# Kernel tuning notes

Measured on AMD Instinct MI355X. Metric: run time of the kernel, lower is better.

The kernel has to match this reference:

```python
import jax, jax.numpy as jnp
import numpy as np


def setup_inputs() -> dict:
    key = jax.random.key(0)
    k1, k2, k3, k4 = jax.random.split(key, 4)
    T, C, D, DY = 8192, 8192, 64, 32
    z_context = jax.random.normal(k1, (C, D), dtype=jnp.float32)
    y_context = jax.random.normal(k2, (C, DY), dtype=jnp.float32)
    z_target = jax.random.normal(k3, (T, D), dtype=jnp.float32)
    # W ~ Uniform(-0.1, 0.1), matching torch init
    W = jax.random.uniform(k4, (D, D), dtype=jnp.float32, minval=-0.1, maxval=0.1)
    return {"z_context": z_context, "y_context": y_context, "z_target": z_target, "W": W}


def _interp(z_context, y_context, z_target, W):
    # score(t,c) = (z_t - z_c)^T W (z_t - z_c), expanded algebraically to avoid
    # the O(T*C*D) pairwise-difference intermediate:
    #   = z_t W z_t + z_c W z_c - z_t W z_c - z_c W z_t
    zt_W = z_target @ W            # (T, D)
    zc_W = z_context @ W           # (C, D)
    q_tt = jnp.sum(zt_W * z_target, axis=-1)   # (T,)
    q_cc = jnp.sum(zc_W * z_context, axis=-1)   # (C,)
    cross = zt_W @ z_context.T + z_target @ zc_W.T  # (T, C): z_t W z_c + z_c W z_t
    scores = q_tt[:, None] + q_cc[None, :] - cross  # (T, C)
    thetas = jnp.exp(-scores)                        # (T, C)
    # weighted sum of context values, normalized per target
    return (thetas @ y_context) / jnp.sum(thetas, axis=-1, keepdims=True)  # (T, DY)


def reference(z_context, y_context, z_target, W):
    return _interp(z_context, y_context, z_target, W)
```

## Files before the change

### kernel.cpp

```cpp
#include <hip/hip_runtime.h>
#include <hip/hip_bf16.h>


typedef float f32x4 __attribute__((ext_vector_type(4)));
typedef __bf16 bf16x8 __attribute__((ext_vector_type(8)));

#define LOG2E 1.4426950408889634f

static __device__ __forceinline__ unsigned short f2bf(float x) {
  unsigned u = __float_as_uint(x);
  u += 0x7fffu + ((u >> 16) & 1u);
  return (unsigned short)(u >> 16);
}
static __device__ __forceinline__ float bf2f(unsigned short h) {
  return __uint_as_float(((unsigned)h) << 16);
}
static __device__ __forceinline__ bf16x8 ldg8(const unsigned short* p) {
  uint4 u = *reinterpret_cast<const uint4*>(p);
  return __builtin_bit_cast(bf16x8, u);
}
static __device__ __forceinline__ unsigned cvt_pk_bf16(float lo, float hi) {
  unsigned r;
  asm("v_cvt_pk_bf16_f32 %0, %1, %2" : "=v"(r) : "v"(lo), "v"(hi));
  return r;
}
static __device__ __forceinline__ void gl2lds(const unsigned short* g, unsigned short* l) {
  __builtin_amdgcn_global_load_lds(
      (const __attribute__((address_space(1))) unsigned int*)g,
      (__attribute__((address_space(3))) unsigned int*)l, 16, 0, 0);
}

__global__ void msym_kernel(const float* __restrict__ W, float* __restrict__ Msym) {
  int idx = blockIdx.x * 256 + threadIdx.x;
  int k = idx >> 6, d = idx & 63;
  Msym[idx] = LOG2E * (W[k * 64 + d] + W[d * 64 + k]);
}

__global__ void prep_kernel(const float* __restrict__ zc, const float* __restrict__ yc,
                            const float* __restrict__ zt, const float* __restrict__ Msym,
                            unsigned short* __restrict__ Qh, unsigned short* __restrict__ Ql,
                            unsigned short* __restrict__ Kh, unsigned short* __restrict__ Kl,
                            unsigned short* __restrict__ Vt, float* __restrict__ bias)
{
  int b = blockIdx.x, tid = threadIdx.x;
  if (b < 2048) {
    int idx = b * 256 + tid;
    int t = idx >> 6, d = idx & 63;
    const float* z = zt + t * 64;
    float q = 0.f;
    #pragma unroll 8
    for (int k = 0; k < 64; ++k) q = fmaf(z[k], Msym[k * 64 + d], q);
    unsigned short h = f2bf(q);
    Qh[idx] = h;
    Ql[idx] = f2bf(q - bf2f(h));
  } else if (b < 4096) {
    int idx = (b - 2048) * 256 + tid;
    float v = zc[idx];
    unsigned short h = f2bf(v);
    Kh[idx] = h;
    Kl[idx] = f2bf(v - bf2f(h));
  } else if (b < 6144) {
    int c = (b - 4096) * 4 + (tid >> 6), j = tid & 63;
    const float* z = zc + c * 64;
    float cs = 0.f;
    #pragma unroll 8
    for (int i = 0; i < 64; ++i) cs = fmaf(z[i], Msym[i * 64 + j], cs);
    float part = cs * z[j];
    #pragma unroll
    for (int off = 32; off >= 1; off >>= 1) part += __shfl_xor(part, off, 64);
    if (j == 0) bias[c] = -0.5f * part;
  } else {
    __shared__ float vt[256][33];
    int cbase = (b - 6144) * 256;
    #pragma unroll
    for (int k = 0; k < 32; ++k) {
      int e = k * 256 + tid;
      vt[e >> 5][e & 31] = yc[cbase * 32 + e];
    }
    __syncthreads();
    #pragma unroll
    for (int k = 0; k < 32; ++k)
      Vt[k * 8192 + cbase + tid] = f2bf(vt[tid][k]);
  }
}


#define STAGE(C0) { \
  const int C0_ = (C0); \
  _Pragma("unroll") \
  for (int i2 = 0; i2 < 2; ++i2) { \
    int i = wid + i2 * 8;                        \
    int row = i * 8 + (lane >> 3); \
    int lchunk = (lane & 7) ^ (lane >> 3); \
    gl2lds(Kh + (C0_ + row) * 64 + lchunk * 8, &KhL[i * 512]); \
    gl2lds(Kl + (C0_ + row) * 64 + lchunk * 8, &KlL[i * 512]); \
  } \
  { \
    int row = wid * 4 + (lane >> 4);             \
    int lchunk = (lane & 15) ^ (row & 15); \
    gl2lds(Vt + row * 8192 + C0_ + lchunk * 8, &VL[wid * 512]); \
  } }

__global__ __launch_bounds__(512, 2) void attn_kernel(
    const unsigned short* __restrict__ Qh, const unsigned short* __restrict__ Ql,
    const unsigned short* __restrict__ Kh, const unsigned short* __restrict__ Kl,
    const unsigned short* __restrict__ Vt, const float* __restrict__ bias,
    float* __restrict__ outAcc, float* __restrict__ denA)
{
  __shared__ unsigned short KhL[128 * 64];
  __shared__ unsigned short KlL[128 * 64];
  __shared__ unsigned short VL[32 * 128];
  __shared__ __align__(16) uint2 p_lds[8][16][34];

  const int tid = threadIdx.x;
  const int wid = tid >> 6, lane = tid & 63;
  const int lr = lane & 15, g = lane >> 4;
  const int tt = blockIdx.x >> 3, cq = blockIdx.x & 7;
  const int tbase = tt * 128 + wid * 16;
  const int cqbase = cq * 1024;

  bf16x8 qh[2], ql[2];
  #pragma unroll
  for (int f = 0; f < 2; ++f) {
    int off = (tbase + lr) * 64 + f * 32 + 8 * g;
    qh[f] = ldg8(Qh + off);
    ql[f] = ldg8(Ql + off);
  }

  uint4 ones_bits = make_uint4(0x3F803F80u, 0x3F803F80u, 0x3F803F80u, 0x3F803F80u);
  bf16x8 vones = __builtin_bit_cast(bf16x8, ones_bits);

  f32x4 acc[2];
  f32x4 den;
  acc[0] = (f32x4)(0.0f);
  acc[1] = (f32x4)(0.0f);
  den = (f32x4)(0.0f);

  for (int st = 0; st < 8; ++st) {
    STAGE(cqbase + st * 128)
    __syncthreads();

    const int cbias = cqbase + st * 128;

    #pragma unroll
    for (int cb = 0; cb < 8; ++cb) {
      int row = cb * 16 + lr;
      int phys0 = g ^ (row & 7);
      int phys1 = (4 + g) ^ (row & 7);
      int off0 = row * 64 + phys0 * 8;
      int off1 = row * 64 + phys1 * 8;
      bf16x8 kh0 = __builtin_bit_cast(bf16x8, *reinterpret_cast<const uint4*>(&KhL[off0]));
      bf16x8 kl0 = __builtin_bit_cast(bf16x8, *reinterpret_cast<const uint4*>(&KlL[off0]));
      bf16x8 kh1 = __builtin_bit_cast(bf16x8, *reinterpret_cast<const uint4*>(&KhL[off1]));
      bf16x8 kl1 = __builtin_bit_cast(bf16x8, *reinterpret_cast<const uint4*>(&KlL[off1]));
      f32x4 sv = (f32x4)(0.0f);
      sv = __builtin_amdgcn_mfma_f32_16x16x32_bf16(kh0, qh[0], sv, 0, 0, 0);
      sv = __builtin_amdgcn_mfma_f32_16x16x32_bf16(kl0, qh[0], sv, 0, 0, 0);
      sv = __builtin_amdgcn_mfma_f32_16x16x32_bf16(kh0, ql[0], sv, 0, 0, 0);
      sv = __builtin_amdgcn_mfma_f32_16x16x32_bf16(kh1, qh[1], sv, 0, 0, 0);
      sv = __builtin_amdgcn_mfma_f32_16x16x32_bf16(kl1, qh[1], sv, 0, 0, 0);
      sv = __builtin_amdgcn_mfma_f32_16x16x32_bf16(kh1, ql[1], sv, 0, 0, 0);
      f32x4 bv = *reinterpret_cast<const f32x4*>(bias + cbias + cb * 16 + 4 * g);
      float p0 = __builtin_amdgcn_exp2f(sv[0] + bv[0]);
      float p1 = __builtin_amdgcn_exp2f(sv[1] + bv[1]);
      float p2 = __builtin_amdgcn_exp2f(sv[2] + bv[2]);
      float p3 = __builtin_amdgcn_exp2f(sv[3] + bv[3]);
      uint2 w2;
      w2.x = cvt_pk_bf16(p0, p1);
      w2.y = cvt_pk_bf16(p2, p3);
      p_lds[wid][lr][cb * 4 + g] = w2;
    }

    #pragma unroll
    for (int ks = 0; ks < 4; ++ks) {
      uint2 ra = p_lds[wid][lr][ks * 8 + 2 * g];
      uint2 rb = p_lds[wid][lr][ks * 8 + 2 * g + 1];
      bf16x8 pa = __builtin_bit_cast(bf16x8, make_uint4(ra.x, ra.y, rb.x, rb.y));
      #pragma unroll
      for (int dyb = 0; dyb < 2; ++dyb) {
        int row = dyb * 16 + lr;
        int phys = (ks * 4 + g) ^ lr;
        bf16x8 vf = __builtin_bit_cast(bf16x8, *reinterpret_cast<const uint4*>(&VL[row * 128 + phys * 8]));
        acc[dyb] = __builtin_amdgcn_mfma_f32_16x16x32_bf16(pa, vf, acc[dyb], 0, 0, 0);
      }
      den = __builtin_amdgcn_mfma_f32_16x16x32_bf16(pa, vones, den, 0, 0, 0);
    }

    __syncthreads();
  }

  #pragma unroll
  for (int dyb = 0; dyb < 2; ++dyb)
    #pragma unroll
    for (int r = 0; r < 4; ++r)
      atomicAdd(&outAcc[(tbase + 4 * g + r) * 32 + dyb * 16 + lr], acc[dyb][r]);
  if (lr == 0) {
    #pragma unroll
    for (int r = 0; r < 4; ++r)
      atomicAdd(&denA[tbase + 4 * g + r], den[r]);
  }
}

__global__ void divide_kernel(float* __restrict__ out, const float* __restrict__ denA)
{
  int i = blockIdx.x * 256 + threadIdx.x;
  out[i] = out[i] / denA[i >> 5];
}

extern "C" void kernel_launch(void* const* d_in, const int* in_sizes, int n_in,
                              void* d_out, int out_size, void* d_ws, size_t ws_size,
                              hipStream_t stream)
{
  const float* zc = (const float*)d_in[0];
  const float* yc = (const float*)d_in[1];
  const float* zt = (const float*)d_in[2];
  const float* W  = (const float*)d_in[3];

  unsigned short* Qh = (unsigned short*)d_ws;
  unsigned short* Ql = Qh + 8192 * 64;
  unsigned short* Kh = Ql + 8192 * 64;
  unsigned short* Kl = Kh + 8192 * 64;
  unsigned short* Vt = Kl + 8192 * 64;
  float* bias = (float*)(Vt + 32 * 8192);
  float* Msym = bias + 8192;
  float* denA = Msym + 4096;
  float* out  = (float*)d_out;

  hipMemsetAsync(out, 0, 8192 * 32 * sizeof(float), stream);
  hipMemsetAsync(denA, 0, 8192 * sizeof(float), stream);
  msym_kernel<<<16, 256, 0, stream>>>(W, Msym);
  prep_kernel<<<6176, 256, 0, stream>>>(zc, yc, zt, Msym, Qh, Ql, Kh, Kl, Vt, bias);
  attn_kernel<<<512, 512, 0, stream>>>(Qh, Ql, Kh, Kl, Vt, bias, out, denA);
  divide_kernel<<<1024, 256, 0, stream>>>(out, denA);
}
```

Before: 72.56 us.

## Switch attention kernel to 32x32 MFMA tiles with register-shuffled probabilities

```diff
diff --git a/kernel.cpp b/kernel.cpp
--- a/kernel.cpp
+++ b/kernel.cpp
@@ -3,6 +3,7 @@
 
 
 typedef float f32x4 __attribute__((ext_vector_type(4)));
+typedef float f32x16 __attribute__((ext_vector_type(16)));
 typedef __bf16 bf16x8 __attribute__((ext_vector_type(8)));
 
 #define LOG2E 1.4426950408889634f
@@ -101,7 +102,7 @@
     gl2lds(Vt + row * 8192 + C0_ + lchunk * 8, &VL[wid * 512]); \
   } }
 
-__global__ __launch_bounds__(512, 2) void attn_kernel(
+__global__ __launch_bounds__(512, 4) void attn_kernel(
     const unsigned short* __restrict__ Qh, const unsigned short* __restrict__ Ql,
     const unsigned short* __restrict__ Kh, const unsigned short* __restrict__ Kl,
     const unsigned short* __restrict__ Vt, const float* __restrict__ bias,
@@ -110,95 +111,112 @@
   __shared__ unsigned short KhL[128 * 64];
   __shared__ unsigned short KlL[128 * 64];
   __shared__ unsigned short VL[32 * 128];
-  __shared__ __align__(16) uint2 p_lds[8][16][34];
 
   const int tid = threadIdx.x;
   const int wid = tid >> 6, lane = tid & 63;
-  const int lr = lane & 15, g = lane >> 4;
-  const int tt = blockIdx.x >> 3, cq = blockIdx.x & 7;
-  const int tbase = tt * 128 + wid * 16;
-  const int cqbase = cq * 1024;
-
-  bf16x8 qh[2], ql[2];
+  const int lm = lane & 31, h = lane >> 5;
+  const int tt = blockIdx.x >> 4, cq = blockIdx.x & 15;
+  const int tbase = tt * 256 + wid * 32;
+  const int cqbase = cq * 512;
+
+  bf16x8 qh[4], ql[4];
   #pragma unroll
-  for (int f = 0; f < 2; ++f) {
-    int off = (tbase + lr) * 64 + f * 32 + 8 * g;
-    qh[f] = ldg8(Qh + off);
-    ql[f] = ldg8(Ql + off);
-  }
-
-  uint4 ones_bits = make_uint4(0x3F803F80u, 0x3F803F80u, 0x3F803F80u, 0x3F803F80u);
-  bf16x8 vones = __builtin_bit_cast(bf16x8, ones_bits);
-
-  f32x4 acc[2];
-  f32x4 den;
-  acc[0] = (f32x4)(0.0f);
-  acc[1] = (f32x4)(0.0f);
-  den = (f32x4)(0.0f);
-
-  for (int st = 0; st < 8; ++st) {
+  for (int kk = 0; kk < 4; ++kk) {
+    int off = (tbase + lm) * 64 + kk * 16 + 8 * h;
+    qh[kk] = ldg8(Qh + off);
+    ql[kk] = ldg8(Ql + off);
+  }
+
+  f32x16 acc = (f32x16)(0.0f);
+  float den = 0.f;
+
+  for (int st = 0; st < 4; ++st) {
     STAGE(cqbase + st * 128)
     __syncthreads();
 
     const int cbias = cqbase + st * 128;
 
     #pragma unroll
-    for (int cb = 0; cb < 8; ++cb) {
-      int row = cb * 16 + lr;
-      int phys0 = g ^ (row & 7);
-      int phys1 = (4 + g) ^ (row & 7);
-      int off0 = row * 64 + phys0 * 8;
-      int off1 = row * 64 + phys1 * 8;
-      bf16x8 kh0 = __builtin_bit_cast(bf16x8, *reinterpret_cast<const uint4*>(&KhL[off0]));
-      bf16x8 kl0 = __builtin_bit_cast(bf16x8, *reinterpret_cast<const uint4*>(&KlL[off0]));
-      bf16x8 kh1 = __builtin_bit_cast(bf16x8, *reinterpret_cast<const uint4*>(&KhL[off1]));
-      bf16x8 kl1 = __builtin_bit_cast(bf16x8, *reinterpret_cast<const uint4*>(&KlL[off1]));
-      f32x4 sv = (f32x4)(0.0f);
-      sv = __builtin_amdgcn_mfma_f32_16x16x32_bf16(kh0, qh[0], sv, 0, 0, 0);
-      sv = __builtin_amdgcn_mfma_f32_16x16x32_bf16(kl0, qh[0], sv, 0, 0, 0);
-      sv = __builtin_amdgcn_mfma_f32_16x16x32_bf16(kh0, ql[0], sv, 0, 0, 0);
-      sv = __builtin_amdgcn_mfma_f32_16x16x32_bf16(kh1, qh[1], sv, 0, 0, 0);
-      sv = __builtin_amdgcn_mfma_f32_16x16x32_bf16(kl1, qh[1], sv, 0, 0, 0);
-      sv = __builtin_amdgcn_mfma_f32_16x16x32_bf16(kh1, ql[1], sv, 0, 0, 0);
-      f32x4 bv = *reinterpret_cast<const f32x4*>(bias + cbias + cb * 16 + 4 * g);
-      float p0 = __builtin_amdgcn_exp2f(sv[0] + bv[0]);
-      float p1 = __builtin_amdgcn_exp2f(sv[1] + bv[1]);
-      float p2 = __builtin_amdgcn_exp2f(sv[2] + bv[2]);
-      float p3 = __builtin_amdgcn_exp2f(sv[3] + bv[3]);
-      uint2 w2;
-      w2.x = cvt_pk_bf16(p0, p1);
-      w2.y = cvt_pk_bf16(p2, p3);
-      p_lds[wid][lr][cb * 4 + g] = w2;
+    for (int cb = 0; cb < 4; ++cb) {
+      const int crow = cb * 32 + lm;
+
+      f32x16 sv = (f32x16)(0.0f);
+      #pragma unroll
+      for (int kk = 0; kk < 4; ++kk) {
+        int phys = (2 * kk + h) ^ (lm & 7);
+        int offr = crow * 64 + phys * 8;
+        bf16x8 kh = __builtin_bit_cast(bf16x8, *reinterpret_cast<const uint4*>(&KhL[offr]));
+        bf16x8 kl = __builtin_bit_cast(bf16x8, *reinterpret_cast<const uint4*>(&KlL[offr]));
+        sv = __builtin_amdgcn_mfma_f32_32x32x16_bf16(kh, qh[kk], sv, 0, 0, 0);
+        sv = __builtin_amdgcn_mfma_f32_32x32x16_bf16(kl, qh[kk], sv, 0, 0, 0);
+        sv = __builtin_amdgcn_mfma_f32_32x32x16_bf16(kh, ql[kk], sv, 0, 0, 0);
+      }
+
+      uint2 own0, own1, own2, own3;
+      float psum;
+      {
+        f32x4 bv0 = *reinterpret_cast<const f32x4*>(bias + cbias + cb * 32 + 0 * 8 + 4 * h);
+        f32x4 bv1 = *reinterpret_cast<const f32x4*>(bias + cbias + cb * 32 + 1 * 8 + 4 * h);
+        f32x4 bv2 = *reinterpret_cast<const f32x4*>(bias + cbias + cb * 32 + 2 * 8 + 4 * h);
+        f32x4 bv3 = *reinterpret_cast<const f32x4*>(bias + cbias + cb * 32 + 3 * 8 + 4 * h);
+        float p00 = __builtin_amdgcn_exp2f(sv[0]  + bv0[0]);
+        float p01 = __builtin_amdgcn_exp2f(sv[1]  + bv0[1]);
+        float p02 = __builtin_amdgcn_exp2f(sv[2]  + bv0[2]);
+        float p03 = __builtin_amdgcn_exp2f(sv[3]  + bv0[3]);
+        float p10 = __builtin_amdgcn_exp2f(sv[4]  + bv1[0]);
+        float p11 = __builtin_amdgcn_exp2f(sv[5]  + bv1[1]);
+        float p12 = __builtin_amdgcn_exp2f(sv[6]  + bv1[2]);
+        float p13 = __builtin_amdgcn_exp2f(sv[7]  + bv1[3]);
+        float p20 = __builtin_amdgcn_exp2f(sv[8]  + bv2[0]);
+        float p21 = __builtin_amdgcn_exp2f(sv[9]  + bv2[1]);
+        float p22 = __builtin_amdgcn_exp2f(sv[10] + bv2[2]);
+        float p23 = __builtin_amdgcn_exp2f(sv[11] + bv2[3]);
+        float p30 = __builtin_amdgcn_exp2f(sv[12] + bv3[0]);
+        float p31 = __builtin_amdgcn_exp2f(sv[13] + bv3[1]);
+        float p32 = __builtin_amdgcn_exp2f(sv[14] + bv3[2]);
+        float p33 = __builtin_amdgcn_exp2f(sv[15] + bv3[3]);
+        psum = ((p00 + p01) + (p02 + p03)) + ((p10 + p11) + (p12 + p13))
+             + ((p20 + p21) + (p22 + p23)) + ((p30 + p31) + (p32 + p33));
+        own0.x = cvt_pk_bf16(p00, p01); own0.y = cvt_pk_bf16(p02, p03);
+        own1.x = cvt_pk_bf16(p10, p11); own1.y = cvt_pk_bf16(p12, p13);
+        own2.x = cvt_pk_bf16(p20, p21); own2.y = cvt_pk_bf16(p22, p23);
+        own3.x = cvt_pk_bf16(p30, p31); own3.y = cvt_pk_bf16(p32, p33);
+      }
+      den += psum;
+
+      unsigned s1x = h ? own0.x : own1.x, s1y = h ? own0.y : own1.y;
+      unsigned s2x = h ? own2.x : own3.x, s2y = h ? own2.y : own3.y;
+      unsigned r1x = __shfl_xor((int)s1x, 32, 64);
+      unsigned r1y = __shfl_xor((int)s1y, 32, 64);
+      unsigned r2x = __shfl_xor((int)s2x, 32, 64);
+      unsigned r2y = __shfl_xor((int)s2y, 32, 64);
+      uint4 f0 = h ? make_uint4(r1x, r1y, own1.x, own1.y)
+                   : make_uint4(own0.x, own0.y, r1x, r1y);
+      uint4 f1 = h ? make_uint4(r2x, r2y, own3.x, own3.y)
+                   : make_uint4(own2.x, own2.y, r2x, r2y);
+
+      {
+        int physv0 = (cb * 4 + 0 * 2 + h) ^ (lm & 15);
+        bf16x8 vf0 = __builtin_bit_cast(bf16x8, *reinterpret_cast<const uint4*>(&VL[lm * 128 + physv0 * 8]));
+        bf16x8 pa0 = __builtin_bit_cast(bf16x8, f0);
+        acc = __builtin_amdgcn_mfma_f32_32x32x16_bf16(pa0, vf0, acc, 0, 0, 0);
+        int physv1 = (cb * 4 + 1 * 2 + h) ^ (lm & 15);
+        bf16x8 vf1 = __builtin_bit_cast(bf16x8, *reinterpret_cast<const uint4*>(&VL[lm * 128 + physv1 * 8]));
+        bf16x8 pa1 = __builtin_bit_cast(bf16x8, f1);
+        acc = __builtin_amdgcn_mfma_f32_32x32x16_bf16(pa1, vf1, acc, 0, 0, 0);
+      }
     }
 
-    #pragma unroll
-    for (int ks = 0; ks < 4; ++ks) {
-      uint2 ra = p_lds[wid][lr][ks * 8 + 2 * g];
-      uint2 rb = p_lds[wid][lr][ks * 8 + 2 * g + 1];
-      bf16x8 pa = __builtin_bit_cast(bf16x8, make_uint4(ra.x, ra.y, rb.x, rb.y));
-      #pragma unroll
-      for (int dyb = 0; dyb < 2; ++dyb) {
-        int row = dyb * 16 + lr;
-        int phys = (ks * 4 + g) ^ lr;
-        bf16x8 vf = __builtin_bit_cast(bf16x8, *reinterpret_cast<const uint4*>(&VL[row * 128 + phys * 8]));
-        acc[dyb] = __builtin_amdgcn_mfma_f32_16x16x32_bf16(pa, vf, acc[dyb], 0, 0, 0);
-      }
-      den = __builtin_amdgcn_mfma_f32_16x16x32_bf16(pa, vones, den, 0, 0, 0);
-    }
-
     __syncthreads();
   }
 
+  den += __shfl_xor(den, 32, 64);
   #pragma unroll
-  for (int dyb = 0; dyb < 2; ++dyb)
-    #pragma unroll
-    for (int r = 0; r < 4; ++r)
-      atomicAdd(&outAcc[(tbase + 4 * g + r) * 32 + dyb * 16 + lr], acc[dyb][r]);
-  if (lr == 0) {
-    #pragma unroll
-    for (int r = 0; r < 4; ++r)
-      atomicAdd(&denA[tbase + 4 * g + r], den[r]);
-  }
+  for (int reg = 0; reg < 16; ++reg) {
+    int trow = (reg & 3) + 8 * (reg >> 2) + 4 * h;
+    atomicAdd(&outAcc[(tbase + trow) * 32 + lm], acc[reg]);
+  }
+  if (lane < 32) atomicAdd(&denA[tbase + lane], den);
 }
 
 __global__ void divide_kernel(float* __restrict__ out, const float* __restrict__ denA)
```

New measurement: 82.30 us. 1.13x slower.
